# Kernel optimization log

Hardware: AMD Instinct MI355X
Metric: run time of the kernel (lower is better)

The kernel has to match this reference:

```python
import jax, jax.numpy as jnp
import numpy as np

B, C, H, W = 64, 3, 64, 64
F = 96          # base_filters
K = 8           # n_mixtures
h, w = H // 2, W // 2
C0 = 2 * C      # channels of each checkerboard half
SECTIONS = [C0, C0, C0 * K, C0 * K, C0 * K]
SPLITS = [int(s) for s in np.cumsum(SECTIONS)[:-1]]
EPS = 1e-6


def conv2d(x, wgt, b):
    y = jax.lax.conv_general_dilated(x, wgt, (1, 1), 'SAME',
                                     dimension_numbers=('NCHW', 'OIHW', 'NCHW'))
    return y + b[None, :, None, None]


def layer_norm(x, g, b, eps=1e-5):
    # nn.LayerNorm(mid_shape): normalize over (C,H,W) per sample
    mu = jnp.mean(x, axis=(1, 2, 3), keepdims=True)
    var = jnp.var(x, axis=(1, 2, 3), keepdims=True)
    return (x - mu) / jnp.sqrt(var + eps) * g[None] + b[None]


def checker_split(z, odd=False):
    Bz, Cz, Hz, Wz = z.shape
    z = z.reshape(Bz, Cz, Hz // 2, 2, Wz // 2, 2)
    p00 = z[:, :, :, 0, :, 0]; p01 = z[:, :, :, 0, :, 1]
    p10 = z[:, :, :, 1, :, 0]; p11 = z[:, :, :, 1, :, 1]
    z0 = jnp.concatenate([p00, p11], axis=1)  # even checkerboard
    z1 = jnp.concatenate([p01, p10], axis=1)  # odd checkerboard
    if odd:
        z0, z1 = z1, z0
    return z0, z1


def checker_merge(z0, z1, odd=False):
    if odd:
        z0, z1 = z1, z0
    Cz = z0.shape[1] // 2
    p00, p11 = z0[:, :Cz], z0[:, Cz:]
    p01, p10 = z1[:, :Cz], z1[:, Cz:]
    Bz, _, hz, wz = p00.shape
    zi = jnp.stack([jnp.stack([p00, p01], axis=-1),
                    jnp.stack([p10, p11], axis=-1)], axis=-2)  # (B,C,h,w,2i,2j)
    z = zi.transpose(0, 1, 2, 4, 3, 5).reshape(Bz, Cz, 2 * hz, 2 * wz)
    return z


def gated_attn(x, qkv_w, qkv_b, proj_w, proj_b):
    Bx, Fx, hx, wx = x.shape
    xf = x.reshape(Bx, Fx, hx * wx).transpose(0, 2, 1)  # (B, L, F)
    qkv = xf @ qkv_w.T + qkv_b
    q, k, v = jnp.split(qkv, 3, axis=-1)
    scores = jnp.einsum('bqf,bkf->bqk', q, k) / jnp.sqrt(jnp.float32(Fx))
    attn = jax.nn.softmax(scores, axis=-1)
    o = jnp.einsum('bqk,bkf->bqf', attn, v)
    g = o @ proj_w.T + proj_b
    ga, gb = jnp.split(g, 2, axis=-1)
    out = xf + ga * jax.nn.sigmoid(gb)  # gated residual
    return out.transpose(0, 2, 1).reshape(Bx, Fx, hx, wx)


def conditioner(z1, conv1_w, conv1_b, gconv_w, gconv_b, ln1_g, ln1_b,
                qkv_w, qkv_b, proj_w, proj_b, ln2_g, ln2_b, conv2_w, conv2_b):
    x = conv2d(z1, conv1_w, conv1_b)
    g = conv2d(x, gconv_w, gconv_b)
    ga, gb = jnp.split(g, 2, axis=1)
    x = x + ga * jax.nn.sigmoid(gb)          # GatedConv2d
    x = layer_norm(x, ln1_g, ln1_b)
    x = gated_attn(x, qkv_w, qkv_b, proj_w, proj_b)
    x = layer_norm(x, ln2_g, ln2_b)
    return conv2d(x, conv2_w, conv2_b)


def _forward(z, log_df_dz, conv1_w, conv1_b, gconv_w, gconv_b, ln1_g, ln1_b,
             qkv_w, qkv_b, proj_w, proj_b, ln2_g, ln2_b, conv2_w, conv2_b,
             a_log_scale, a_bias):
    z0, z1 = checker_split(z)
    params = conditioner(z1, conv1_w, conv1_b, gconv_w, gconv_b, ln1_g, ln1_b,
                         qkv_w, qkv_b, proj_w, proj_b, ln2_g, ln2_b, conv2_w, conv2_b)
    a, b, logpi, mu, s = jnp.split(params, SPLITS, axis=1)
    a = jnp.tanh(a) * a_log_scale + a_bias
    Bz = z0.shape[0]
    logpi = jax.nn.log_softmax(logpi.reshape(Bz, K, C0, h, w), axis=1)
    mu = mu.reshape(Bz, K, C0, h, w)
    s = s.reshape(Bz, K, C0, h, w)
    # mixture-of-logistics CDF
    u = (z0[:, None] - mu) * jnp.exp(-s)
    x = jnp.sum(jnp.exp(logpi) * jax.nn.sigmoid(u), axis=1)
    log_pdf = jax.scipy.special.logsumexp(
        logpi - s + jax.nn.log_sigmoid(u) + jax.nn.log_sigmoid(-u), axis=1)
    log_df_dz = log_df_dz + jnp.sum(log_pdf.reshape(Bz, -1), axis=1)
    # logit transform
    x = jnp.clip(x, EPS, 1.0 - EPS)
    z0n = jnp.log(x) - jnp.log1p(-x)
    log_df_dz = log_df_dz + jnp.sum((-jnp.log(x) - jnp.log1p(-x)).reshape(Bz, -1), axis=1)
    # affine rescale
    z0n = z0n * jnp.exp(a) + b
    log_df_dz = log_df_dz + jnp.sum(a.reshape(Bz, -1), axis=1)
    return checker_merge(z0n, z1), log_df_dz


def setup_inputs() -> dict:
    key = jax.random.key(0)
    ks = jax.random.split(key, 10)
    sc = 0.05
    return dict(
        z=jax.random.normal(ks[0], (B, C, H, W), jnp.float32),
        log_df_dz=jnp.zeros((B,), jnp.float32),
        conv1_w=sc * jax.random.normal(ks[1], (F, C0, 3, 3), jnp.float32),
        conv1_b=jnp.zeros((F,), jnp.float32),
        gconv_w=sc * jax.random.normal(ks[2], (2 * F, F, 3, 3), jnp.float32),
        gconv_b=jnp.zeros((2 * F,), jnp.float32),
        ln1_g=jnp.ones((F, h, w), jnp.float32),
        ln1_b=jnp.zeros((F, h, w), jnp.float32),
        qkv_w=sc * jax.random.normal(ks[3], (3 * F, F), jnp.float32),
        qkv_b=jnp.zeros((3 * F,), jnp.float32),
        proj_w=sc * jax.random.normal(ks[4], (2 * F, F), jnp.float32),
        proj_b=jnp.zeros((2 * F,), jnp.float32),
        ln2_g=jnp.ones((F, h, w), jnp.float32),
        ln2_b=jnp.zeros((F, h, w), jnp.float32),
        conv2_w=sc * jax.random.normal(ks[5], (sum(SECTIONS), F, 3, 3), jnp.float32),
        conv2_b=jnp.zeros((sum(SECTIONS),), jnp.float32),
        a_log_scale=0.01 * jax.random.normal(ks[6], (1,), jnp.float32),
        a_bias=0.01 * jax.random.normal(ks[7], (1,), jnp.float32),
    )


def reference(z, log_df_dz, conv1_w, conv1_b, gconv_w, gconv_b, ln1_g, ln1_b,
              qkv_w, qkv_b, proj_w, proj_b, ln2_g, ln2_b, conv2_w, conv2_b,
              a_log_scale, a_bias):
    return _forward(z, log_df_dz, conv1_w, conv1_b, gconv_w, gconv_b, ln1_g, ln1_b,
                    qkv_w, qkv_b, proj_w, proj_b, ln2_g, ln2_b, conv2_w, conv2_b,
                    a_log_scale, a_bias)
```

## Files before the change

kernel.cpp:

```cpp
#include <hip/hip_runtime.h>
#include <cstdint>
#include <cstddef>


typedef unsigned short u16;
typedef __attribute__((ext_vector_type(8))) short short8;
typedef __attribute__((ext_vector_type(4))) float f32x4;
typedef __attribute__((ext_vector_type(4))) unsigned int u32x4;

__device__ __forceinline__ float sigm(float x){ return 1.0f/(1.0f+__expf(-x)); }

__device__ __forceinline__ u16 f2bf(float f){
    unsigned int u = __float_as_uint(f);
    u += 0x7fffu + ((u >> 16) & 1u);
    return (u16)(u >> 16);
}
__device__ __forceinline__ float bf2f(u16 v){
    unsigned int u = ((unsigned int)v) << 16;
    return __uint_as_float(u);
}

__device__ __forceinline__ void dma16(const u16* g, u16* l){
    __builtin_amdgcn_global_load_lds(
        (const __attribute__((address_space(1))) void*)g,
        (__attribute__((address_space(3))) void*)l,
        16, 0, 0);
}

__device__ __forceinline__ float ex2(float x){
    float r; asm("v_exp_f32 %0, %1" : "=v"(r) : "v"(x)); return r;
}
__device__ __forceinline__ unsigned cvtpk(float lo, float hi){
    unsigned r; asm("v_cvt_pk_bf16_f32 %0, %1, %2" : "=v"(r) : "v"(lo), "v"(hi)); return r;
}
__device__ __forceinline__ void plswap32(unsigned &a, unsigned &b){
    asm("v_permlane32_swap_b32 %0, %1" : "+v"(a), "+v"(b));
}
__device__ __forceinline__ void plswap16(unsigned &a, unsigned &b){
    asm("v_permlane16_swap_b32 %0, %1" : "+v"(a), "+v"(b));
}

#define SOFTPACK(S, LACC, PA) do { \
    unsigned pk_[4][2]; \
    _Pragma("unroll") \
    for (int t=0;t<4;++t){ \
        float e0 = ex2(S[t][0]); \
        float e1 = ex2(S[t][1]); \
        float e2 = ex2(S[t][2]); \
        float e3 = ex2(S[t][3]); \
        LACC += (e0+e1)+(e2+e3); \
        pk_[t][0] = cvtpk(e0,e1); \
        pk_[t][1] = cvtpk(e2,e3); \
    } \
    _Pragma("unroll") \
    for (int kk=0;kk<2;++kk){ \
        unsigned a0 = pk_[2*kk][0], b0 = pk_[2*kk+1][0]; \
        unsigned a1 = pk_[2*kk][1], b1 = pk_[2*kk+1][1]; \
        plswap32(a0,b0); plswap16(a0,b0); \
        plswap32(a1,b1); plswap16(a1,b1); \
        u32x4 dw_; dw_[0]=a0; dw_[1]=a1; dw_[2]=b0; dw_[3]=b1; \
        PA[kk] = __builtin_bit_cast(short8, dw_); \
    } \
} while(0)

__device__ __forceinline__ short8 ln_frag(const u16* __restrict__ xg,
    const float* __restrict__ gt, const float* __restrict__ bt,
    int p, int c0, float mu, float rr)
{
    short8 x8 = *reinterpret_cast<const short8*>(xg + (size_t)p*96 + c0);
    const float* gp = gt + (size_t)p*96 + c0;
    const float* bp = bt + (size_t)p*96 + c0;
    short8 o;
    #pragma unroll
    for (int j=0;j<8;++j){
        float ag = rr*gp[j];
        o[j] = (short)f2bf(bf2f((u16)x8[j])*ag + (bp[j] - mu*ag));
    }
    return o;
}

__global__ __launch_bounds__(256) void k_prep(
    const float* __restrict__ z, const float* __restrict__ c1w, const float* __restrict__ c1b,
    const float* __restrict__ gw, const float* __restrict__ c2w,
    const float* __restrict__ qkvw, const float* __restrict__ pw,
    const float* __restrict__ ln1g, const float* __restrict__ ln1b,
    const float* __restrict__ ln2g, const float* __restrict__ ln2b,
    const float* __restrict__ logdf,
    u16* __restrict__ x1b,
    u16* __restrict__ Wg, u16* __restrict__ W2,
    u16* __restrict__ Wqkv, u16* __restrict__ Wproj,
    float* __restrict__ gt1, float* __restrict__ bt1,
    float* __restrict__ gt2, float* __restrict__ bt2,
    float* __restrict__ outlog)
{
    int blk = blockIdx.x;
    int tid = threadIdx.x;
    __shared__ float tin[6][6][34];
    __shared__ __align__(16) u16 Wc[96][72];
    __shared__ __align__(16) u16 imc[128][72];

    if (blk < 512){
        int b  = blk >> 3;
        int pg = blk & 7;
        int r0 = pg*4;
        for (int e = tid; e < 96*72; e += 256){
            int oc = e/72, k = e%72;
            Wc[oc][k] = (k < 54) ? f2bf(c1w[oc*54 + k]) : (u16)0;
        }
        for (int idx = tid; idx < 6*6*34; idx += 256){
            int c = idx/204, rem = idx%204;
            int rr = rem/34, q = rem%34;
            int ii = r0 - 1 + rr, jj = q - 1;
            float v = 0.f;
            if ((unsigned)ii < 32u && (unsigned)jj < 32u){
                if (c < 3) v = z[((b*3+c)*64 + 2*ii)*64 + (2*jj+1)];
                else       v = z[((b*3+(c-3))*64 + (2*ii+1))*64 + 2*jj];
            }
            tin[c][rr][q] = v;
        }
        __syncthreads();
        for (int e = tid; e < 128*72; e += 256){
            int px = e/72, k = e%72;
            float v = 0.f;
            if (k < 54){
                int c = k/9, rr = (k%9)/3, dcc = k%3;
                v = tin[c][(px>>5)+rr][(px&31)+dcc];
            }
            imc[px][k] = f2bf(v);
        }
        __syncthreads();

        int w = tid >> 6, lane = tid & 63;
        int cc = lane & 15, gg = lane >> 4;
        f32x4 acc[2][6];
        #pragma unroll
        for (int u=0;u<2;++u)
            #pragma unroll
            for (int t=0;t<6;++t) acc[u][t] = (f32x4){0.f,0.f,0.f,0.f};

        #pragma unroll
        for (int ks=0; ks<2; ++ks){
            short8 a0 = *reinterpret_cast<const short8*>(&imc[w*32 + cc     ][ks*32 + 8*gg]);
            short8 a1 = *reinterpret_cast<const short8*>(&imc[w*32 + 16 + cc][ks*32 + 8*gg]);
            #pragma unroll
            for (int t=0; t<6; ++t){
                short8 bb = *reinterpret_cast<const short8*>(&Wc[t*16+cc][ks*32 + 8*gg]);
                acc[0][t] = __builtin_amdgcn_mfma_f32_16x16x32_bf16(a0, bb, acc[0][t], 0,0,0);
                acc[1][t] = __builtin_amdgcn_mfma_f32_16x16x32_bf16(a1, bb, acc[1][t], 0,0,0);
            }
        }

        #pragma unroll
        for (int u=0;u<2;++u){
            int p0 = pg*128 + w*32 + u*16 + gg*4;
            #pragma unroll
            for (int t=0;t<6;++t){
                int oc = t*16+cc;
                float bv = c1b[oc];
                #pragma unroll
                for (int r=0;r<4;++r)
                    x1b[((size_t)(b*1024) + p0 + r)*96 + oc] = f2bf(acc[u][t][r] + bv);
            }
        }
    } else if (blk < 1160){
        int idx = (blk-512)*256 + tid;
        int j = idx & 7;
        int lane = (idx >> 3) & 63;
        int fo = idx >> 9;
        int frag = fo % 18;
        int tob = fo / 18;
        int obk = tob & 1, tap = tob >> 1;
        int t = frag/3, ks = frag%3;
        int cc = lane & 15, gg = lane >> 4;
        int ocp = obk*96 + t*16 + cc;
        int r2 = ocp%96, isB = r2/48, i2 = r2%48;
        int oc = (ocp/96)*48 + i2 + isB*96;
        int ic = ks*32 + 8*gg + j;
        Wg[idx] = f2bf(gw[(size_t)(oc*96+ic)*9 + tap]);
    } else if (blk < 1700){
        int idx = (blk-1160)*256 + tid;
        int j = idx & 7;
        int lane = (idx >> 3) & 63;
        int fo = idx >> 9;
        int frag = fo % 15;
        int tob = fo / 15;
        int obk = tob & 1, tap = tob >> 1;
        int t = frag/3, ks = frag%3;
        int cc = lane & 15, gg = lane >> 4;
        int oc = obk*80 + t*16 + cc;
        int ic = ks*32 + 8*gg + j;
        W2[idx] = (oc < 156) ? f2bf(c2w[(size_t)(oc*96+ic)*9 + tap]) : (u16)0;
    } else if (blk < 1808){
        int idx = (blk-1700)*256 + tid;
        int j = idx & 7;
        int lane = (idx >> 3) & 63;
        int fo = idx >> 9;
        int frag = fo % 27;
        int obk = fo / 27;
        int t = frag/3, ks = frag%3;
        int cc = lane & 15, gg = lane >> 4;
        int n = obk*144 + t*16 + cc;
        int ic = ks*32 + 8*gg + j;
        Wqkv[idx] = f2bf(qkvw[(size_t)n*96 + ic]);
    } else if (blk < 1880){
        int idx = (blk-1808)*256 + tid;
        int j = idx & 7;
        int lane = (idx >> 3) & 63;
        int fo = idx >> 9;
        int frag = fo % 18;
        int obk = fo / 18;
        int t = frag/3, ks = frag%3;
        int cc = lane & 15, gg = lane >> 4;
        int ocp = obk*96 + t*16 + cc;
        int r2 = ocp%96, isB = r2/48, i2 = r2%48;
        int oc = obk*48 + i2 + isB*96;
        int ic = ks*32 + 8*gg + j;
        Wproj[idx] = f2bf(pw[(size_t)oc*96 + ic]);
    } else if (blk < 2264){
        int idx = (blk-1880)*256 + tid;
        int c = idx >> 10, p = idx & 1023;
        gt1[p*96 + c] = ln1g[idx];
    } else if (blk < 2648){
        int idx = (blk-2264)*256 + tid;
        int c = idx >> 10, p = idx & 1023;
        bt1[p*96 + c] = ln1b[idx];
    } else if (blk < 3032){
        int idx = (blk-2648)*256 + tid;
        int c = idx >> 10, p = idx & 1023;
        gt2[p*96 + c] = ln2g[idx];
    } else if (blk < 3416){
        int idx = (blk-3032)*256 + tid;
        int c = idx >> 10, p = idx & 1023;
        bt2[p*96 + c] = ln2b[idx];
    } else {
        if (tid < 64) outlog[tid] = logdf[tid];
    }
}

__global__ __launch_bounds__(256,4) void k_gconv(const u16* __restrict__ Xpb,
    const u16* __restrict__ Wt, const float* __restrict__ bias,
    u16* __restrict__ outb, float* __restrict__ partials)
{
    int blk  = blockIdx.x;
    int obk  = blk & 1;
    int pblk = (blk >> 1) & 7;
    int b    = blk >> 4;
    int tid  = threadIdx.x;
    int w = tid >> 6, lane = tid & 63;
    int cc = lane & 15, gg = lane >> 4;

    __shared__ __align__(16) u16 Ws[2][9216];
    __shared__ float red[8];

    f32x4 acc[2][6];
    #pragma unroll
    for (int u=0;u<2;++u)
        #pragma unroll
        for (int t=0;t<6;++t) acc[u][t] = (f32x4){0.f,0.f,0.f,0.f};

    int base = pblk*128 + w*32;
    int ia = base >> 5;
    const u16* xb = Xpb + (size_t)b*1024*96;

    {
        const u16* src = Wt + (size_t)obk*9216;
        #pragma unroll
        for (int i=0;i<5;++i){
            int c = tid + 256*i;
            if (c < 1152) dma16(src + (size_t)c*8, Ws[0] + (size_t)(w*64+256*i)*8);
        }
    }

    for (int tap=0; tap<9; ++tap){
        __syncthreads();
        if (tap < 8){
            const u16* src = Wt + (size_t)((tap+1)*2 + obk)*9216;
            int nb = (tap+1)&1;
            #pragma unroll
            for (int i=0;i<5;++i){
                int c = tid + 256*i;
                if (c < 1152) dma16(src + (size_t)c*8, Ws[nb] + (size_t)(w*64+256*i)*8);
            }
        }
        const u16* Wc = Ws[tap&1];
        int dr = tap/3 - 1, dc = tap%3 - 1;

        int ii = ia + dr;
        int jj0 = cc + dc, jj1 = cc + 16 + dc;
        bool rv = ((unsigned)ii < 32u);
        bool v0 = rv && ((unsigned)jj0 < 32u);
        bool v1 = rv && ((unsigned)jj1 < 32u);
        const u16* ar0 = xb + (ptrdiff_t)(ii*32 + jj0)*96 + 8*gg;
        const u16* ar1 = xb + (ptrdiff_t)(ii*32 + jj1)*96 + 8*gg;

        #pragma unroll
        for (int ks=0; ks<3; ++ks){
            short8 a0 = {0,0,0,0,0,0,0,0};
            short8 a1 = {0,0,0,0,0,0,0,0};
            if (v0) a0 = *reinterpret_cast<const short8*>(ar0 + ks*32);
            if (v1) a1 = *reinterpret_cast<const short8*>(ar1 + ks*32);
            #pragma unroll
            for (int t=0; t<6; ++t){
                short8 bb = *reinterpret_cast<const short8*>(Wc + ((size_t)(t*3+ks)*64 + lane)*8);
                acc[0][t] = __builtin_amdgcn_mfma_f32_16x16x32_bf16(a0, bb, acc[0][t], 0,0,0);
                acc[1][t] = __builtin_amdgcn_mfma_f32_16x16x32_bf16(a1, bb, acc[1][t], 0,0,0);
            }
        }
    }

    float s = 0.f, ssq = 0.f;
    #pragma unroll
    for (int u=0;u<2;++u){
        int p0 = base + u*16 + gg*4;
        #pragma unroll
        for (int t=0;t<3;++t){
            int ocA = obk*48 + t*16+cc;
            float ba = bias[ocA], bbv = bias[ocA+96];
            #pragma unroll
            for (int r=0;r<4;++r){
                float res = bf2f(Xpb[((size_t)b*1024 + p0+r)*96 + ocA]);
                float va = acc[u][t][r]   + ba;
                float vb = acc[u][t+3][r] + bbv;
                float v = res + va*sigm(vb);
                outb[((size_t)b*1024 + p0+r)*96 + ocA] = f2bf(v);
                s += v; ssq += v*v;
            }
        }
    }
    #pragma unroll
    for (int o=32;o>0;o>>=1){ s += __shfl_down(s,o,64); ssq += __shfl_down(ssq,o,64); }
    if (lane==0){ red[w]=s; red[4+w]=ssq; }
    __syncthreads();
    if (tid==0){
        int slot = b*16 + pblk*2 + obk;
        partials[slot*2+0] = red[0]+red[1]+red[2]+red[3];
        partials[slot*2+1] = red[4]+red[5]+red[6]+red[7];
    }
}

__global__ __launch_bounds__(256) void k_lne(const u16* __restrict__ xb,
    const float* __restrict__ gt, const float* __restrict__ bt,
    const float* __restrict__ partials, u16* __restrict__ out)
{
    int b = blockIdx.x / 48, rem = blockIdx.x % 48;
    float s=0.f, ss=0.f;
    #pragma unroll
    for (int i=0;i<16;++i){ s += partials[(b*16+i)*2]; ss += partials[(b*16+i)*2+1]; }
    float mu = s/98304.f;
    float r = rsqrtf(ss/98304.f - mu*mu + 1e-5f);

    int e8 = rem*256 + threadIdx.x;
    size_t base = (size_t)b*98304 + (size_t)e8*8;
    short8 x8 = *reinterpret_cast<const short8*>(xb + base);
    const float* gp = gt + e8*8;
    const float* bp = bt + e8*8;
    short8 o8;
    #pragma unroll
    for (int i=0;i<8;++i)
        o8[i] = (short)f2bf((bf2f((u16)x8[i]) - mu)*r*gp[i] + bp[i]);
    *reinterpret_cast<short8*>(out + base) = o8;
}

__global__ __launch_bounds__(256,4) void k_conv2m(const u16* __restrict__ Xpb,
    const u16* __restrict__ Wt, const float* __restrict__ bias,
    u16* __restrict__ out)
{
    int blk  = blockIdx.x;
    int obk  = blk & 1;
    int pblk = (blk >> 1) & 7;
    int b    = blk >> 4;
    int tid  = threadIdx.x;
    int w = tid >> 6, lane = tid & 63;
    int cc = lane & 15, gg = lane >> 4;

    __shared__ __align__(16) u16 Ws[2][7680];

    f32x4 acc[2][5];
    #pragma unroll
    for (int u=0;u<2;++u)
        #pragma unroll
        for (int t=0;t<5;++t) acc[u][t] = (f32x4){0.f,0.f,0.f,0.f};

    int base = pblk*128 + w*32;
    int ia = base >> 5;
    const u16* xb = Xpb + (size_t)b*1024*96;

    {
        const u16* src = Wt + (size_t)obk*7680;
        #pragma unroll
        for (int i=0;i<4;++i){
            int c = tid + 256*i;
            if (c < 960) dma16(src + (size_t)c*8, Ws[0] + (size_t)(w*64+256*i)*8);
        }
    }

    for (int tap=0; tap<9; ++tap){
        __syncthreads();
        if (tap < 8){
            const u16* src = Wt + (size_t)((tap+1)*2 + obk)*7680;
            int nb = (tap+1)&1;
            #pragma unroll
            for (int i=0;i<4;++i){
                int c = tid + 256*i;
                if (c < 960) dma16(src + (size_t)c*8, Ws[nb] + (size_t)(w*64+256*i)*8);
            }
        }
        const u16* Wc = Ws[tap&1];
        int dr = tap/3 - 1, dc = tap%3 - 1;

        int ii = ia + dr;
        int jj0 = cc + dc, jj1 = cc + 16 + dc;
        bool rv = ((unsigned)ii < 32u);
        bool v0 = rv && ((unsigned)jj0 < 32u);
        bool v1 = rv && ((unsigned)jj1 < 32u);
        const u16* ar0 = xb + (ptrdiff_t)(ii*32 + jj0)*96 + 8*gg;
        const u16* ar1 = xb + (ptrdiff_t)(ii*32 + jj1)*96 + 8*gg;

        #pragma unroll
        for (int ks=0; ks<3; ++ks){
            short8 a0 = {0,0,0,0,0,0,0,0};
            short8 a1 = {0,0,0,0,0,0,0,0};
            if (v0) a0 = *reinterpret_cast<const short8*>(ar0 + ks*32);
            if (v1) a1 = *reinterpret_cast<const short8*>(ar1 + ks*32);
            #pragma unroll
            for (int t=0; t<5; ++t){
                short8 bb = *reinterpret_cast<const short8*>(Wc + ((size_t)(t*3+ks)*64 + lane)*8);
                acc[0][t] = __builtin_amdgcn_mfma_f32_16x16x32_bf16(a0, bb, acc[0][t], 0,0,0);
                acc[1][t] = __builtin_amdgcn_mfma_f32_16x16x32_bf16(a1, bb, acc[1][t], 0,0,0);
            }
        }
    }

    #pragma unroll
    for (int u=0;u<2;++u){
        int p0 = base + u*16 + gg*4;
        #pragma unroll
        for (int t=0;t<5;++t){
            int oc = obk*80 + t*16+cc;
            if (oc < 156){
                float bv = bias[oc];
                u16* op = out + ((size_t)b*156 + oc)*1024 + p0;
                #pragma unroll
                for (int r=0;r<4;++r) op[r] = f2bf(acc[u][t][r] + bv);
            }
        }
    }
}

__global__ __launch_bounds__(256,4) void k_qkvm(const u16* __restrict__ Xg,
    const float* __restrict__ gt, const float* __restrict__ bt,
    const float* __restrict__ part,
    const u16* __restrict__ Wt, const float* __restrict__ bias,
    u16* __restrict__ Qb, u16* __restrict__ Kf, u16* __restrict__ Vf)
{
    int blk  = blockIdx.x;
    int obk  = blk & 1;
    int pblk = (blk >> 1) & 7;
    int b    = blk >> 4;
    int tid  = threadIdx.x;
    int w = tid >> 6, lane = tid & 63;
    int cc = lane & 15, gg = lane >> 4;
    const float scale = 0.14724445f;

    __shared__ __align__(16) u16 Ws[13824];
    {
        const u16* src = Wt + (size_t)obk*13824;
        #pragma unroll
        for (int i=0;i<7;++i){
            int c = tid + 256*i;
            if (c < 1728) dma16(src + (size_t)c*8, Ws + (size_t)(w*64+256*i)*8);
        }
    }

    float sS=0.f, sQ=0.f;
    #pragma unroll
    for (int i=0;i<16;++i){ sS += part[(b*16+i)*2]; sQ += part[(b*16+i)*2+1]; }
    float mu = sS/98304.f;
    float rr = rsqrtf(sQ/98304.f - mu*mu + 1e-5f);

    f32x4 acc[2][9];
    #pragma unroll
    for (int u=0;u<2;++u)
        #pragma unroll
        for (int t=0;t<9;++t) acc[u][t] = (f32x4){0.f,0.f,0.f,0.f};

    int base = pblk*128 + w*32;
    const u16* xg = Xg + (size_t)b*1024*96;
    __syncthreads();

    #pragma unroll
    for (int ks=0; ks<3; ++ks){
        int c0 = ks*32 + 8*gg;
        short8 a0 = ln_frag(xg, gt, bt, base+cc,    c0, mu, rr);
        short8 a1 = ln_frag(xg, gt, bt, base+cc+16, c0, mu, rr);
        #pragma unroll
        for (int t=0; t<9; ++t){
            short8 bb = *reinterpret_cast<const short8*>(Ws + ((size_t)(t*3+ks)*64 + lane)*8);
            acc[0][t] = __builtin_amdgcn_mfma_f32_16x16x32_bf16(a0, bb, acc[0][t], 0,0,0);
            acc[1][t] = __builtin_amdgcn_mfma_f32_16x16x32_bf16(a1, bb, acc[1][t], 0,0,0);
        }
    }

    #pragma unroll
    for (int u=0;u<2;++u){
        int p0 = base + u*16 + gg*4;
        #pragma unroll
        for (int t=0;t<9;++t){
            int n = obk*144 + t*16+cc;
            float bv = bias[n];
            #pragma unroll
            for (int r=0;r<4;++r){
                int p = p0 + r;
                float av = acc[u][t][r] + bv;
                if (n < 96){
                    Qb[((size_t)(b*1024+p))*96 + n] = f2bf(av*scale);
                } else if (n < 192){
                    int f = n-96;
                    int jt = p>>6, t16 = (p>>4)&3, ccs = p&15;
                    int ks = f>>5, ggs = (f>>3)&3, j = f&7;
                    Kf[(size_t)(b*16+jt)*6144 + (size_t)(((t16*3+ks)*4+ggs)*16+ccs)*8 + j] = f2bf(av);
                } else {
                    int f = n-192;
                    int jt = p>>6, kl = p&63;
                    int kk = kl>>5, ggs = (kl>>3)&3, j = kl&7;
                    int ft = f>>4, ccs = f&15;
                    Vf[(size_t)(b*16+jt)*6144 + (size_t)(((ft*2+kk)*4+ggs)*16+ccs)*8 + j] = f2bf(av);
                }
            }
        }
    }
}

__global__ __launch_bounds__(256,2) void k_attn(const u16* __restrict__ Qb,
    const u16* __restrict__ Kf, const u16* __restrict__ Vf, u16* __restrict__ Ob)
{
    int qt = blockIdx.x >> 6;
    int b  = blockIdx.x & 63;
    int tid = threadIdx.x;
    int w  = tid >> 6;
    int lane = tid & 63;
    int cc = lane & 15;
    int gg = lane >> 4;

    __shared__ __align__(16) u16 Ks[2][6144];
    __shared__ __align__(16) u16 Vs[2][6144];

    int q0 = qt*128 + w*32;

    short8 qf[2][3];
    {
        const u16* qr0 = Qb + ((size_t)(b*1024 + q0 + cc))*96;
        #pragma unroll
        for (int ks=0; ks<3; ++ks){
            qf[0][ks] = *reinterpret_cast<const short8*>(qr0 + ks*32 + 8*gg);
            qf[1][ks] = *reinterpret_cast<const short8*>(qr0 + (size_t)16*96 + ks*32 + 8*gg);
        }
    }

    f32x4 Oacc[2][6];
    #pragma unroll
    for (int u=0;u<2;++u)
        #pragma unroll
        for (int ft=0; ft<6; ++ft) Oacc[u][ft] = (f32x4){0.f,0.f,0.f,0.f};
    float l_acc[2] = {0.f, 0.f};

    const u16* Kb0 = Kf + (size_t)(b*16)*6144;
    const u16* Vb0 = Vf + (size_t)(b*16)*6144;

    #pragma unroll
    for (int i=0;i<3;++i){
        size_t c8 = (size_t)(tid + 256*i)*8;
        size_t l8 = (size_t)(w*64 + 256*i)*8;
        dma16(Kb0 + c8, Ks[0] + l8);
        dma16(Vb0 + c8, Vs[0] + l8);
    }

    for (int jt=0; jt<16; ++jt){
        __syncthreads();
        if (jt < 15){
            const u16* kn = Kb0 + (size_t)(jt+1)*6144;
            const u16* vn = Vb0 + (size_t)(jt+1)*6144;
            int nb = (jt+1)&1;
            #pragma unroll
            for (int i=0;i<3;++i){
                size_t c8 = (size_t)(tid + 256*i)*8;
                size_t l8 = (size_t)(w*64 + 256*i)*8;
                dma16(kn + c8, Ks[nb] + l8);
                dma16(vn + c8, Vs[nb] + l8);
            }
        }

        const u16* Kc = Ks[jt&1];
        const u16* Vc = Vs[jt&1];

        f32x4 S0[4], S1[4];
        #pragma unroll
        for (int t=0;t<4;++t){ S0[t] = (f32x4){0.f,0.f,0.f,0.f}; S1[t] = (f32x4){0.f,0.f,0.f,0.f}; }

        __builtin_amdgcn_s_setprio(1);
        #pragma unroll
        for (int ks=0; ks<3; ++ks){
            #pragma unroll
            for (int t=0; t<4; ++t){
                short8 kb = *reinterpret_cast<const short8*>(Kc + ((t*3+ks)*64 + lane)*8);
                S0[t] = __builtin_amdgcn_mfma_f32_16x16x32_bf16(kb, qf[0][ks], S0[t], 0,0,0);
                S1[t] = __builtin_amdgcn_mfma_f32_16x16x32_bf16(kb, qf[1][ks], S1[t], 0,0,0);
            }
        }
        __builtin_amdgcn_s_setprio(0);

        short8 pa0[2], pa1[2];
        SOFTPACK(S0, l_acc[0], pa0);
        SOFTPACK(S1, l_acc[1], pa1);

        __builtin_amdgcn_s_setprio(1);
        #pragma unroll
        for (int kk=0; kk<2; ++kk){
            #pragma unroll
            for (int ft=0; ft<6; ++ft){
                short8 vb = *reinterpret_cast<const short8*>(Vc + ((ft*2+kk)*64 + lane)*8);
                Oacc[0][ft] = __builtin_amdgcn_mfma_f32_16x16x32_bf16(pa0[kk], vb, Oacc[0][ft], 0,0,0);
                Oacc[1][ft] = __builtin_amdgcn_mfma_f32_16x16x32_bf16(pa1[kk], vb, Oacc[1][ft], 0,0,0);
            }
        }
        __builtin_amdgcn_s_setprio(0);
    }

    #pragma unroll
    for (int u=0;u<2;++u){
        float lv = l_acc[u];
        lv += __shfl_xor(lv, 16, 64);
        lv += __shfl_xor(lv, 32, 64);
        float linv[4];
        #pragma unroll
        for (int r=0;r<4;++r) linv[r] = 1.0f / __shfl(lv, 4*gg + r, 64);
        #pragma unroll
        for (int ft=0; ft<6; ++ft)
            #pragma unroll
            for (int r=0; r<4; ++r)
                Ob[((size_t)(b*1024 + q0 + u*16 + 4*gg + r))*96 + ft*16 + cc]
                    = f2bf(Oacc[u][ft][r]*linv[r]);
    }
}

__global__ __launch_bounds__(256,4) void k_projm(const u16* __restrict__ Opb,
    const u16* __restrict__ Wt, const float* __restrict__ bias,
    const u16* __restrict__ Xg, const float* __restrict__ gt, const float* __restrict__ bt,
    const float* __restrict__ part1,
    u16* __restrict__ outb, float* __restrict__ partials)
{
    int blk  = blockIdx.x;
    int obk  = blk & 1;
    int pblk = (blk >> 1) & 7;
    int b    = blk >> 4;
    int tid  = threadIdx.x;
    int w = tid >> 6, lane = tid & 63;
    int cc = lane & 15, gg = lane >> 4;

    __shared__ __align__(16) u16 Ws[9216];
    __shared__ float red[8];
    {
        const u16* src = Wt + (size_t)obk*9216;
        #pragma unroll
        for (int i=0;i<5;++i){
            int c = tid + 256*i;
            if (c < 1152) dma16(src + (size_t)c*8, Ws + (size_t)(w*64+256*i)*8);
        }
    }

    float sS=0.f, sQ=0.f;
    #pragma unroll
    for (int i=0;i<16;++i){ sS += part1[(b*16+i)*2]; sQ += part1[(b*16+i)*2+1]; }
    float mu1 = sS/98304.f;
    float rr1 = rsqrtf(sQ/98304.f - mu1*mu1 + 1e-5f);

    f32x4 acc[2][6];
    #pragma unroll
    for (int u=0;u<2;++u)
        #pragma unroll
        for (int t=0;t<6;++t) acc[u][t] = (f32x4){0.f,0.f,0.f,0.f};

    int base = pblk*128 + w*32;
    const u16* xb = Opb + ((size_t)b*1024 + base)*96;
    __syncthreads();

    #pragma unroll
    for (int ks=0; ks<3; ++ks){
        short8 a0 = *reinterpret_cast<const short8*>(xb + (size_t)cc*96      + ks*32 + 8*gg);
        short8 a1 = *reinterpret_cast<const short8*>(xb + (size_t)(cc+16)*96 + ks*32 + 8*gg);
        #pragma unroll
        for (int t=0; t<6; ++t){
            short8 bb = *reinterpret_cast<const short8*>(Ws + ((size_t)(t*3+ks)*64 + lane)*8);
            acc[0][t] = __builtin_amdgcn_mfma_f32_16x16x32_bf16(a0, bb, acc[0][t], 0,0,0);
            acc[1][t] = __builtin_amdgcn_mfma_f32_16x16x32_bf16(a1, bb, acc[1][t], 0,0,0);
        }
    }

    const u16* resb = Xg + (size_t)b*1024*96;
    float s = 0.f, ssq = 0.f;
    #pragma unroll
    for (int u=0;u<2;++u){
        int p0 = base + u*16 + gg*4;
        #pragma unroll
        for (int t=0;t<3;++t){
            int ocA = obk*48 + t*16+cc;
            float ba = bias[ocA], bbv = bias[ocA+96];
            #pragma unroll
            for (int r=0;r<4;++r){
                int pl = p0 + r;
                float ga = acc[u][t][r]   + ba;
                float gb = acc[u][t+3][r] + bbv;
                float xv = bf2f(resb[(size_t)pl*96 + ocA]);
                float res = (xv - mu1)*rr1*gt[(size_t)pl*96 + ocA] + bt[(size_t)pl*96 + ocA];
                float v = res + ga * sigm(gb);
                outb[((size_t)b*1024 + pl)*96 + ocA] = f2bf(v);
                s += v; ssq += v*v;
            }
        }
    }
    #pragma unroll
    for (int o=32;o>0;o>>=1){ s += __shfl_down(s,o,64); ssq += __shfl_down(ssq,o,64); }
    if (lane==0){ red[w]=s; red[4+w]=ssq; }
    __syncthreads();
    if (tid==0){
        int slot = b*16 + pblk*2 + obk;
        partials[slot*2+0] = red[0]+red[1]+red[2]+red[3];
        partials[slot*2+1] = red[4]+red[5]+red[6]+red[7];
    }
}

__global__ __launch_bounds__(256) void k_mix(const float* __restrict__ z,
    const u16* __restrict__ params, const float* __restrict__ a_ls_p,
    const float* __restrict__ a_b_p, float* __restrict__ out_z, float* __restrict__ out_log)
{
    int b = blockIdx.x / 24;
    int rem = blockIdx.x % 24;
    int c0 = rem / 4;
    int pix = (rem & 3)*256 + threadIdx.x;
    int i = pix >> 5, j = pix & 31;
    float als = a_ls_p[0], abv = a_b_p[0];
    const u16* pb = params + (size_t)b*156*1024;
    float logacc = 0.f;

    if (c0 < 3){
        int idx01 = ((b*3+c0)*64 + 2*i)*64 + 2*j+1;
        int idx10 = ((b*3+c0)*64 + 2*i+1)*64 + 2*j;
        out_z[idx01] = z[idx01];
        out_z[idx10] = z[idx10];
    }

    {
        float z0v = (c0<3) ? z[((b*3+c0)*64 + 2*i)*64 + 2*j]
                           : z[((b*3+(c0-3))*64 + 2*i+1)*64 + 2*j+1];
        float a_raw = bf2f(pb[(c0)*1024 + pix]);
        float bco   = bf2f(pb[(6+c0)*1024 + pix]);
        float lp[8], mu[8], sv[8];
        float m1 = -1e30f;
        #pragma unroll
        for (int k=0;k<8;++k){
            lp[k] = bf2f(pb[(12 + k*6 + c0)*1024 + pix]);
            mu[k] = bf2f(pb[(60 + k*6 + c0)*1024 + pix]);
            sv[k] = bf2f(pb[(108 + k*6 + c0)*1024 + pix]);
            m1 = fmaxf(m1, lp[k]);
        }
        float se = 0.f;
        #pragma unroll
        for (int k=0;k<8;++k) se += __expf(lp[k]-m1);
        float lse = m1 + __logf(se);
        float xm = 0.f, mt = -1e30f;
        float t[8];
        #pragma unroll
        for (int k=0;k<8;++k){
            float lpn = lp[k] - lse;
            float u = (z0v - mu[k]) * __expf(-sv[k]);
            float au = fabsf(u);
            xm += __expf(lpn) * (1.f/(1.f+__expf(-u)));
            float lss = -(au + 2.f*log1pf(__expf(-au)));
            float tk = lpn - sv[k] + lss;
            t[k] = tk; mt = fmaxf(mt, tk);
        }
        float se2 = 0.f;
        #pragma unroll
        for (int k=0;k<8;++k) se2 += __expf(t[k]-mt);
        logacc += mt + __logf(se2);
        xm = fminf(fmaxf(xm, 1e-6f), 1.f-1e-6f);
        float lx = __logf(xm), l1x = log1pf(-xm);
        logacc += -lx - l1x;
        float aa = tanhf(a_raw)*als + abv;
        float z0n = (lx - l1x)*__expf(aa) + bco;
        logacc += aa;
        int oidx = (c0<3) ? ((b*3+c0)*64 + 2*i)*64 + 2*j
                          : ((b*3+(c0-3))*64 + 2*i+1)*64 + 2*j+1;
        out_z[oidx] = z0n;
    }

    #pragma unroll
    for (int o=32;o>0;o>>=1) logacc += __shfl_down(logacc, o, 64);
    __shared__ float part[4];
    if ((threadIdx.x&63)==0) part[threadIdx.x>>6] = logacc;
    __syncthreads();
    if (threadIdx.x==0){
        atomicAdd(out_log + b, part[0]+part[1]+part[2]+part[3]);
    }
}

extern "C" void kernel_launch(void* const* d_in, const int* in_sizes, int n_in,
                              void* d_out, int out_size, void* d_ws, size_t ws_size,
                              hipStream_t stream)
{
    const float* z     = (const float*)d_in[0];
    const float* logdf = (const float*)d_in[1];
    const float* c1w   = (const float*)d_in[2];
    const float* c1b   = (const float*)d_in[3];
    const float* gw    = (const float*)d_in[4];
    const float* gcb   = (const float*)d_in[5];
    const float* ln1g  = (const float*)d_in[6];
    const float* ln1b  = (const float*)d_in[7];
    const float* qkvw  = (const float*)d_in[8];
    const float* qkvb  = (const float*)d_in[9];
    const float* pw    = (const float*)d_in[10];
    const float* pbb   = (const float*)d_in[11];
    const float* ln2g  = (const float*)d_in[12];
    const float* ln2b  = (const float*)d_in[13];
    const float* c2w   = (const float*)d_in[14];
    const float* c2b   = (const float*)d_in[15];
    const float* als   = (const float*)d_in[16];
    const float* ab    = (const float*)d_in[17];

    float* out_z   = (float*)d_out;
    float* out_log = out_z + 786432;

    float* ws     = (float*)d_ws;
    u16*   x1b    = (u16*)(ws + 0);
    u16*   xg_b   = (u16*)(ws + 3145728);
    u16*   Kf     = (u16*)(ws + 6291456);
    u16*   Vf     = (u16*)(ws + 9437184);
    u16*   Ob     = (u16*)(ws + 12582912);
    u16*   x2b    = (u16*)(ws + 15728640);
    u16*   Qb     = x1b;
    u16*   xln2b  = Kf;
    u16*   params = (u16*)(ws + 9437184);
    const size_t T = 19660800;
    float* gt1    = ws + T;
    float* bt1    = ws + T + 98304;
    float* gt2    = ws + T + 196608;
    float* bt2    = ws + T + 294912;
    float* part1  = ws + T + 393216;
    float* part2  = ws + T + 395264;
    u16*   Wg     = (u16*)(ws + T + 397568);
    u16*   W2     = (u16*)(ws + T + 480512);
    u16*   Wqkv   = (u16*)(ws + T + 549632);
    u16*   Wproj  = (u16*)(ws + T + 563456);

    k_prep   <<<3417, 256, 0, stream>>>(z, c1w, c1b, gw, c2w, qkvw, pw,
                                        ln1g, ln1b, ln2g, ln2b, logdf,
                                        x1b, Wg, W2, Wqkv, Wproj,
                                        gt1, bt1, gt2, bt2, out_log);
    k_gconv  <<<1024, 256, 0, stream>>>(x1b, Wg, gcb, xg_b, part1);
    k_qkvm   <<<1024, 256, 0, stream>>>(xg_b, gt1, bt1, part1, Wqkv, qkvb, Qb, Kf, Vf);
    k_attn   <<<512, 256, 0, stream>>>(Qb, Kf, Vf, Ob);
    k_projm  <<<1024, 256, 0, stream>>>(Ob, Wproj, pbb, xg_b, gt1, bt1, part1, x2b, part2);
    k_lne    <<<3072, 256, 0, stream>>>(x2b, gt2, bt2, part2, xln2b);
    k_conv2m <<<1024, 256, 0, stream>>>(xln2b, W2, c2b, params);
    k_mix    <<<1536, 256, 0, stream>>>(z, params, als, ab, out_z, out_log);
}
```

Measured before the change: 268.6 us.

## Merge per-stage kernels into two cooperative persistent kernels with grid sync

The seven non-attention stage kernels are turned into device functions and grouped into two persistent cooperative kernels of 1024 blocks that step through the phases with grid-wide barriers. The aim is to cut kernel launch overhead and the gaps between dependent stages. Shared memory becomes one manually carved buffer per block. If the cooperative launch fails, the code falls back to separate per-phase launches. The costs are grid-sync overhead and lower occupancy freedom, because the grid is capped at the co-resident block count.

```diff
diff --git a/kernel.cpp b/kernel.cpp
--- a/kernel.cpp
+++ b/kernel.cpp
@@ -1,6 +1,9 @@
 #include <hip/hip_runtime.h>
+#include <hip/hip_cooperative_groups.h>
 #include <cstdint>
 #include <cstddef>
+
+namespace cg = cooperative_groups;
 
 
 typedef unsigned short u16;
@@ -79,33 +82,32 @@
     return o;
 }
 
-__global__ __launch_bounds__(256) void k_prep(
-    const float* __restrict__ z, const float* __restrict__ c1w, const float* __restrict__ c1b,
-    const float* __restrict__ gw, const float* __restrict__ c2w,
-    const float* __restrict__ qkvw, const float* __restrict__ pw,
-    const float* __restrict__ ln1g, const float* __restrict__ ln1b,
-    const float* __restrict__ ln2g, const float* __restrict__ ln2b,
-    const float* __restrict__ logdf,
-    u16* __restrict__ x1b,
-    u16* __restrict__ Wg, u16* __restrict__ W2,
-    u16* __restrict__ Wqkv, u16* __restrict__ Wproj,
-    float* __restrict__ gt1, float* __restrict__ bt1,
-    float* __restrict__ gt2, float* __restrict__ bt2,
-    float* __restrict__ outlog)
-{
-    int blk = blockIdx.x;
+struct PArgs {
+    const float *z, *c1w, *c1b, *gw, *c2w, *qkvw, *pw;
+    const float *ln1g, *ln1b, *ln2g, *ln2b, *logdf;
+    const float *gcb, *qkvb, *pbb, *c2b, *als, *ab;
+    u16 *x1b, *Wg, *W2, *Wqkv, *Wproj;
+    float *gt1, *bt1, *gt2, *bt2, *part1, *part2;
+    u16 *xg_b, *Qb, *Kf, *Vf, *Ob, *x2b, *xln2b, *params;
+    float *out_z, *out_log;
+};
+
+
+__device__ void prep_unit(int blk, const PArgs& a, unsigned char* smem)
+{
     int tid = threadIdx.x;
-    __shared__ float tin[6][6][34];
-    __shared__ __align__(16) u16 Wc[96][72];
-    __shared__ __align__(16) u16 imc[128][72];
+    float (*tin)[6][34] = (float(*)[6][34])(smem);
+    u16   (*Wc)[72]     = (u16(*)[72])(smem + 4896);
+    u16   (*imc)[72]    = (u16(*)[72])(smem + 4896 + 13824);
 
     if (blk < 512){
+        __syncthreads();
         int b  = blk >> 3;
         int pg = blk & 7;
         int r0 = pg*4;
         for (int e = tid; e < 96*72; e += 256){
             int oc = e/72, k = e%72;
-            Wc[oc][k] = (k < 54) ? f2bf(c1w[oc*54 + k]) : (u16)0;
+            Wc[oc][k] = (k < 54) ? f2bf(a.c1w[oc*54 + k]) : (u16)0;
         }
         for (int idx = tid; idx < 6*6*34; idx += 256){
             int c = idx/204, rem = idx%204;
@@ -113,8 +115,8 @@
             int ii = r0 - 1 + rr, jj = q - 1;
             float v = 0.f;
             if ((unsigned)ii < 32u && (unsigned)jj < 32u){
-                if (c < 3) v = z[((b*3+c)*64 + 2*ii)*64 + (2*jj+1)];
-                else       v = z[((b*3+(c-3))*64 + (2*ii+1))*64 + 2*jj];
+                if (c < 3) v = a.z[((b*3+c)*64 + 2*ii)*64 + (2*jj+1)];
+                else       v = a.z[((b*3+(c-3))*64 + (2*ii+1))*64 + 2*jj];
             }
             tin[c][rr][q] = v;
         }
@@ -156,10 +158,10 @@
             #pragma unroll
             for (int t=0;t<6;++t){
                 int oc = t*16+cc;
-                float bv = c1b[oc];
+                float bv = a.c1b[oc];
                 #pragma unroll
                 for (int r=0;r<4;++r)
-                    x1b[((size_t)(b*1024) + p0 + r)*96 + oc] = f2bf(acc[u][t][r] + bv);
+                    a.x1b[((size_t)(b*1024) + p0 + r)*96 + oc] = f2bf(acc[u][t][r] + bv);
             }
         }
     } else if (blk < 1160){
@@ -176,7 +178,7 @@
         int r2 = ocp%96, isB = r2/48, i2 = r2%48;
         int oc = (ocp/96)*48 + i2 + isB*96;
         int ic = ks*32 + 8*gg + j;
-        Wg[idx] = f2bf(gw[(size_t)(oc*96+ic)*9 + tap]);
+        a.Wg[idx] = f2bf(a.gw[(size_t)(oc*96+ic)*9 + tap]);
     } else if (blk < 1700){
         int idx = (blk-1160)*256 + tid;
         int j = idx & 7;
@@ -189,7 +191,7 @@
         int cc = lane & 15, gg = lane >> 4;
         int oc = obk*80 + t*16 + cc;
         int ic = ks*32 + 8*gg + j;
-        W2[idx] = (oc < 156) ? f2bf(c2w[(size_t)(oc*96+ic)*9 + tap]) : (u16)0;
+        a.W2[idx] = (oc < 156) ? f2bf(a.c2w[(size_t)(oc*96+ic)*9 + tap]) : (u16)0;
     } else if (blk < 1808){
         int idx = (blk-1700)*256 + tid;
         int j = idx & 7;
@@ -201,7 +203,7 @@
         int cc = lane & 15, gg = lane >> 4;
         int n = obk*144 + t*16 + cc;
         int ic = ks*32 + 8*gg + j;
-        Wqkv[idx] = f2bf(qkvw[(size_t)n*96 + ic]);
+        a.Wqkv[idx] = f2bf(a.qkvw[(size_t)n*96 + ic]);
     } else if (blk < 1880){
         int idx = (blk-1808)*256 + tid;
         int j = idx & 7;
@@ -215,33 +217,30 @@
         int r2 = ocp%96, isB = r2/48, i2 = r2%48;
         int oc = obk*48 + i2 + isB*96;
         int ic = ks*32 + 8*gg + j;
-        Wproj[idx] = f2bf(pw[(size_t)oc*96 + ic]);
+        a.Wproj[idx] = f2bf(a.pw[(size_t)oc*96 + ic]);
     } else if (blk < 2264){
         int idx = (blk-1880)*256 + tid;
         int c = idx >> 10, p = idx & 1023;
-        gt1[p*96 + c] = ln1g[idx];
+        a.gt1[p*96 + c] = a.ln1g[idx];
     } else if (blk < 2648){
         int idx = (blk-2264)*256 + tid;
         int c = idx >> 10, p = idx & 1023;
-        bt1[p*96 + c] = ln1b[idx];
+        a.bt1[p*96 + c] = a.ln1b[idx];
     } else if (blk < 3032){
         int idx = (blk-2648)*256 + tid;
         int c = idx >> 10, p = idx & 1023;
-        gt2[p*96 + c] = ln2g[idx];
+        a.gt2[p*96 + c] = a.ln2g[idx];
     } else if (blk < 3416){
         int idx = (blk-3032)*256 + tid;
         int c = idx >> 10, p = idx & 1023;
-        bt2[p*96 + c] = ln2b[idx];
+        a.bt2[p*96 + c] = a.ln2b[idx];
     } else {
-        if (tid < 64) outlog[tid] = logdf[tid];
-    }
-}
-
-__global__ __launch_bounds__(256,4) void k_gconv(const u16* __restrict__ Xpb,
-    const u16* __restrict__ Wt, const float* __restrict__ bias,
-    u16* __restrict__ outb, float* __restrict__ partials)
-{
-    int blk  = blockIdx.x;
+        if (tid < 64) a.out_log[tid] = a.logdf[tid];
+    }
+}
+
+__device__ void gconv_unit(int blk, const PArgs& a, unsigned char* smem)
+{
     int obk  = blk & 1;
     int pblk = (blk >> 1) & 7;
     int b    = blk >> 4;
@@ -249,8 +248,9 @@
     int w = tid >> 6, lane = tid & 63;
     int cc = lane & 15, gg = lane >> 4;
 
-    __shared__ __align__(16) u16 Ws[2][9216];
-    __shared__ float red[8];
+    u16* Ws0 = (u16*)smem;
+    u16* Ws1 = (u16*)(smem + 18432);
+    float* red = (float*)(smem + 36864);
 
     f32x4 acc[2][6];
     #pragma unroll
@@ -260,29 +260,30 @@
 
     int base = pblk*128 + w*32;
     int ia = base >> 5;
-    const u16* xb = Xpb + (size_t)b*1024*96;
+    const u16* xb = a.xg_b;
+    xb = a.x1b + (size_t)b*1024*96;
 
     {
-        const u16* src = Wt + (size_t)obk*9216;
+        const u16* src = a.Wg + (size_t)obk*9216;
         #pragma unroll
         for (int i=0;i<5;++i){
             int c = tid + 256*i;
-            if (c < 1152) dma16(src + (size_t)c*8, Ws[0] + (size_t)(w*64+256*i)*8);
+            if (c < 1152) dma16(src + (size_t)c*8, Ws0 + (size_t)(w*64+256*i)*8);
         }
     }
 
     for (int tap=0; tap<9; ++tap){
         __syncthreads();
         if (tap < 8){
-            const u16* src = Wt + (size_t)((tap+1)*2 + obk)*9216;
-            int nb = (tap+1)&1;
+            const u16* src = a.Wg + (size_t)((tap+1)*2 + obk)*9216;
+            u16* dst = ((tap+1)&1) ? Ws1 : Ws0;
             #pragma unroll
             for (int i=0;i<5;++i){
                 int c = tid + 256*i;
-                if (c < 1152) dma16(src + (size_t)c*8, Ws[nb] + (size_t)(w*64+256*i)*8);
-            }
-        }
-        const u16* Wc = Ws[tap&1];
+                if (c < 1152) dma16(src + (size_t)c*8, dst + (size_t)(w*64+256*i)*8);
+            }
+        }
+        const u16* Wc = (tap&1) ? Ws1 : Ws0;
         int dr = tap/3 - 1, dc = tap%3 - 1;
 
         int ii = ia + dr;
@@ -315,14 +316,14 @@
         #pragma unroll
         for (int t=0;t<3;++t){
             int ocA = obk*48 + t*16+cc;
-            float ba = bias[ocA], bbv = bias[ocA+96];
+            float ba = a.gcb[ocA], bbv = a.gcb[ocA+96];
             #pragma unroll
             for (int r=0;r<4;++r){
-                float res = bf2f(Xpb[((size_t)b*1024 + p0+r)*96 + ocA]);
+                float res = bf2f(a.x1b[((size_t)b*1024 + p0+r)*96 + ocA]);
                 float va = acc[u][t][r]   + ba;
                 float vb = acc[u][t+3][r] + bbv;
                 float v = res + va*sigm(vb);
-                outb[((size_t)b*1024 + p0+r)*96 + ocA] = f2bf(v);
+                a.xg_b[((size_t)b*1024 + p0+r)*96 + ocA] = f2bf(v);
                 s += v; ssq += v*v;
             }
         }
@@ -333,47 +334,203 @@
     __syncthreads();
     if (tid==0){
         int slot = b*16 + pblk*2 + obk;
-        partials[slot*2+0] = red[0]+red[1]+red[2]+red[3];
-        partials[slot*2+1] = red[4]+red[5]+red[6]+red[7];
-    }
-}
-
-__global__ __launch_bounds__(256) void k_lne(const u16* __restrict__ xb,
-    const float* __restrict__ gt, const float* __restrict__ bt,
-    const float* __restrict__ partials, u16* __restrict__ out)
-{
-    int b = blockIdx.x / 48, rem = blockIdx.x % 48;
-    float s=0.f, ss=0.f;
-    #pragma unroll
-    for (int i=0;i<16;++i){ s += partials[(b*16+i)*2]; ss += partials[(b*16+i)*2+1]; }
-    float mu = s/98304.f;
-    float r = rsqrtf(ss/98304.f - mu*mu + 1e-5f);
-
-    int e8 = rem*256 + threadIdx.x;
-    size_t base = (size_t)b*98304 + (size_t)e8*8;
-    short8 x8 = *reinterpret_cast<const short8*>(xb + base);
-    const float* gp = gt + e8*8;
-    const float* bp = bt + e8*8;
-    short8 o8;
-    #pragma unroll
-    for (int i=0;i<8;++i)
-        o8[i] = (short)f2bf((bf2f((u16)x8[i]) - mu)*r*gp[i] + bp[i]);
-    *reinterpret_cast<short8*>(out + base) = o8;
-}
-
-__global__ __launch_bounds__(256,4) void k_conv2m(const u16* __restrict__ Xpb,
-    const u16* __restrict__ Wt, const float* __restrict__ bias,
-    u16* __restrict__ out)
-{
-    int blk  = blockIdx.x;
+        a.part1[slot*2+0] = red[0]+red[1]+red[2]+red[3];
+        a.part1[slot*2+1] = red[4]+red[5]+red[6]+red[7];
+    }
+}
+
+__device__ void qkvm_unit(int blk, const PArgs& a, unsigned char* smem)
+{
     int obk  = blk & 1;
     int pblk = (blk >> 1) & 7;
     int b    = blk >> 4;
     int tid  = threadIdx.x;
     int w = tid >> 6, lane = tid & 63;
     int cc = lane & 15, gg = lane >> 4;
-
-    __shared__ __align__(16) u16 Ws[2][7680];
+    const float scale = 0.14724445f;
+
+    u16* Ws = (u16*)smem;
+    {
+        const u16* src = a.Wqkv + (size_t)obk*13824;
+        #pragma unroll
+        for (int i=0;i<7;++i){
+            int c = tid + 256*i;
+            if (c < 1728) dma16(src + (size_t)c*8, Ws + (size_t)(w*64+256*i)*8);
+        }
+    }
+
+    float sS=0.f, sQ=0.f;
+    #pragma unroll
+    for (int i=0;i<16;++i){ sS += a.part1[(b*16+i)*2]; sQ += a.part1[(b*16+i)*2+1]; }
+    float mu = sS/98304.f;
+    float rr = rsqrtf(sQ/98304.f - mu*mu + 1e-5f);
+
+    f32x4 acc[2][9];
+    #pragma unroll
+    for (int u=0;u<2;++u)
+        #pragma unroll
+        for (int t=0;t<9;++t) acc[u][t] = (f32x4){0.f,0.f,0.f,0.f};
+
+    int base = pblk*128 + w*32;
+    const u16* xg = a.xg_b + (size_t)b*1024*96;
+    __syncthreads();
+
+    #pragma unroll
+    for (int ks=0; ks<3; ++ks){
+        int c0 = ks*32 + 8*gg;
+        short8 a0 = ln_frag(xg, a.gt1, a.bt1, base+cc,    c0, mu, rr);
+        short8 a1 = ln_frag(xg, a.gt1, a.bt1, base+cc+16, c0, mu, rr);
+        #pragma unroll
+        for (int t=0; t<9; ++t){
+            short8 bb = *reinterpret_cast<const short8*>(Ws + ((size_t)(t*3+ks)*64 + lane)*8);
+            acc[0][t] = __builtin_amdgcn_mfma_f32_16x16x32_bf16(a0, bb, acc[0][t], 0,0,0);
+            acc[1][t] = __builtin_amdgcn_mfma_f32_16x16x32_bf16(a1, bb, acc[1][t], 0,0,0);
+        }
+    }
+
+    #pragma unroll
+    for (int u=0;u<2;++u){
+        int p0 = base + u*16 + gg*4;
+        #pragma unroll
+        for (int t=0;t<9;++t){
+            int n = obk*144 + t*16+cc;
+            float bv = a.qkvb[n];
+            #pragma unroll
+            for (int r=0;r<4;++r){
+                int p = p0 + r;
+                float av = acc[u][t][r] + bv;
+                if (n < 96){
+                    a.Qb[((size_t)(b*1024+p))*96 + n] = f2bf(av*scale);
+                } else if (n < 192){
+                    int f = n-96;
+                    int jt = p>>6, t16 = (p>>4)&3, ccs = p&15;
+                    int ks = f>>5, ggs = (f>>3)&3, j = f&7;
+                    a.Kf[(size_t)(b*16+jt)*6144 + (size_t)(((t16*3+ks)*4+ggs)*16+ccs)*8 + j] = f2bf(av);
+                } else {
+                    int f = n-192;
+                    int jt = p>>6, kl = p&63;
+                    int kk = kl>>5, ggs = (kl>>3)&3, j = kl&7;
+                    int ft = f>>4, ccs = f&15;
+                    a.Vf[(size_t)(b*16+jt)*6144 + (size_t)(((ft*2+kk)*4+ggs)*16+ccs)*8 + j] = f2bf(av);
+                }
+            }
+        }
+    }
+}
+
+__device__ void projm_unit(int blk, const PArgs& a, unsigned char* smem)
+{
+    int obk  = blk & 1;
+    int pblk = (blk >> 1) & 7;
+    int b    = blk >> 4;
+    int tid  = threadIdx.x;
+    int w = tid >> 6, lane = tid & 63;
+    int cc = lane & 15, gg = lane >> 4;
+
+    u16* Ws = (u16*)smem;
+    float* red = (float*)(smem + 18432);
+    {
+        const u16* src = a.Wproj + (size_t)obk*9216;
+        #pragma unroll
+        for (int i=0;i<5;++i){
+            int c = tid + 256*i;
+            if (c < 1152) dma16(src + (size_t)c*8, Ws + (size_t)(w*64+256*i)*8);
+        }
+    }
+
+    float sS=0.f, sQ=0.f;
+    #pragma unroll
+    for (int i=0;i<16;++i){ sS += a.part1[(b*16+i)*2]; sQ += a.part1[(b*16+i)*2+1]; }
+    float mu1 = sS/98304.f;
+    float rr1 = rsqrtf(sQ/98304.f - mu1*mu1 + 1e-5f);
+
+    f32x4 acc[2][6];
+    #pragma unroll
+    for (int u=0;u<2;++u)
+        #pragma unroll
+        for (int t=0;t<6;++t) acc[u][t] = (f32x4){0.f,0.f,0.f,0.f};
+
+    int base = pblk*128 + w*32;
+    const u16* xb = a.Ob + ((size_t)b*1024 + base)*96;
+    __syncthreads();
+
+    #pragma unroll
+    for (int ks=0; ks<3; ++ks){
+        short8 a0 = *reinterpret_cast<const short8*>(xb + (size_t)cc*96      + ks*32 + 8*gg);
+        short8 a1 = *reinterpret_cast<const short8*>(xb + (size_t)(cc+16)*96 + ks*32 + 8*gg);
+        #pragma unroll
+        for (int t=0; t<6; ++t){
+            short8 bb = *reinterpret_cast<const short8*>(Ws + ((size_t)(t*3+ks)*64 + lane)*8);
+            acc[0][t] = __builtin_amdgcn_mfma_f32_16x16x32_bf16(a0, bb, acc[0][t], 0,0,0);
+            acc[1][t] = __builtin_amdgcn_mfma_f32_16x16x32_bf16(a1, bb, acc[1][t], 0,0,0);
+        }
+    }
+
+    const u16* resb = a.xg_b + (size_t)b*1024*96;
+    float s = 0.f, ssq = 0.f;
+    #pragma unroll
+    for (int u=0;u<2;++u){
+        int p0 = base + u*16 + gg*4;
+        #pragma unroll
+        for (int t=0;t<3;++t){
+            int ocA = obk*48 + t*16+cc;
+            float ba = a.pbb[ocA], bbv = a.pbb[ocA+96];
+            #pragma unroll
+            for (int r=0;r<4;++r){
+                int pl = p0 + r;
+                float ga = acc[u][t][r]   + ba;
+                float gb = acc[u][t+3][r] + bbv;
+                float xv = bf2f(resb[(size_t)pl*96 + ocA]);
+                float res = (xv - mu1)*rr1*a.gt1[(size_t)pl*96 + ocA] + a.bt1[(size_t)pl*96 + ocA];
+                float v = res + ga * sigm(gb);
+                a.x2b[((size_t)b*1024 + pl)*96 + ocA] = f2bf(v);
+                s += v; ssq += v*v;
+            }
+        }
+    }
+    #pragma unroll
+    for (int o=32;o>0;o>>=1){ s += __shfl_down(s,o,64); ssq += __shfl_down(ssq,o,64); }
+    if (lane==0){ red[w]=s; red[4+w]=ssq; }
+    __syncthreads();
+    if (tid==0){
+        int slot = b*16 + pblk*2 + obk;
+        a.part2[slot*2+0] = red[0]+red[1]+red[2]+red[3];
+        a.part2[slot*2+1] = red[4]+red[5]+red[6]+red[7];
+    }
+}
+
+__device__ void lne2_unit(int u, const PArgs& a)
+{
+    int b = u / 48, rem = u % 48;
+    float s=0.f, ss=0.f;
+    #pragma unroll
+    for (int i=0;i<16;++i){ s += a.part2[(b*16+i)*2]; ss += a.part2[(b*16+i)*2+1]; }
+    float mu = s/98304.f;
+    float r = rsqrtf(ss/98304.f - mu*mu + 1e-5f);
+
+    int e8 = rem*256 + threadIdx.x;
+    size_t base = (size_t)b*98304 + (size_t)e8*8;
+    short8 x8 = *reinterpret_cast<const short8*>(a.x2b + base);
+    const float* gp = a.gt2 + e8*8;
+    const float* bp = a.bt2 + e8*8;
+    short8 o8;
+    #pragma unroll
+    for (int i=0;i<8;++i)
+        o8[i] = (short)f2bf((bf2f((u16)x8[i]) - mu)*r*gp[i] + bp[i]);
+    *reinterpret_cast<short8*>(a.xln2b + base) = o8;
+}
+
+__device__ void conv2m_unit(int blk, const PArgs& a, unsigned char* smem)
+{
+    int obk  = blk & 1;
+    int pblk = (blk >> 1) & 7;
+    int b    = blk >> 4;
+    int tid  = threadIdx.x;
+    int w = tid >> 6, lane = tid & 63;
+    int cc = lane & 15, gg = lane >> 4;
+
+    u16* Ws0 = (u16*)smem;
+    u16* Ws1 = (u16*)(smem + 15360);
 
     f32x4 acc[2][5];
     #pragma unroll
@@ -383,29 +540,29 @@
 
     int base = pblk*128 + w*32;
     int ia = base >> 5;
-    const u16* xb = Xpb + (size_t)b*1024*96;
+    const u16* xb = a.xln2b + (size_t)b*1024*96;
 
     {
-        const u16* src = Wt + (size_t)obk*7680;
+        const u16* src = a.W2 + (size_t)obk*7680;
         #pragma unroll
         for (int i=0;i<4;++i){
             int c = tid + 256*i;
-            if (c < 960) dma16(src + (size_t)c*8, Ws[0] + (size_t)(w*64+256*i)*8);
+            if (c < 960) dma16(src + (size_t)c*8, Ws0 + (size_t)(w*64+256*i)*8);
         }
     }
 
     for (int tap=0; tap<9; ++tap){
         __syncthreads();
         if (tap < 8){
-            const u16* src = Wt + (size_t)((tap+1)*2 + obk)*7680;
-            int nb = (tap+1)&1;
+            const u16* src = a.W2 + (size_t)((tap+1)*2 + obk)*7680;
+            u16* dst = ((tap+1)&1) ? Ws1 : Ws0;
             #pragma unroll
             for (int i=0;i<4;++i){
                 int c = tid + 256*i;
-                if (c < 960) dma16(src + (size_t)c*8, Ws[nb] + (size_t)(w*64+256*i)*8);
-            }
-        }
-        const u16* Wc = Ws[tap&1];
+                if (c < 960) dma16(src + (size_t)c*8, dst + (size_t)(w*64+256*i)*8);
+            }
+        }
+        const u16* Wc = (tap&1) ? Ws1 : Ws0;
         int dr = tap/3 - 1, dc = tap%3 - 1;
 
         int ii = ia + dr;
@@ -438,8 +595,8 @@
         for (int t=0;t<5;++t){
             int oc = obk*80 + t*16+cc;
             if (oc < 156){
-                float bv = bias[oc];
-                u16* op = out + ((size_t)b*156 + oc)*1024 + p0;
+                float bv = a.c2b[oc];
+                u16* op = a.params + ((size_t)b*156 + oc)*1024 + p0;
                 #pragma unroll
                 for (int r=0;r<4;++r) op[r] = f2bf(acc[u][t][r] + bv);
             }
@@ -447,87 +604,117 @@
     }
 }
 
-__global__ __launch_bounds__(256,4) void k_qkvm(const u16* __restrict__ Xg,
-    const float* __restrict__ gt, const float* __restrict__ bt,
-    const float* __restrict__ part,
-    const u16* __restrict__ Wt, const float* __restrict__ bias,
-    u16* __restrict__ Qb, u16* __restrict__ Kf, u16* __restrict__ Vf)
-{
-    int blk  = blockIdx.x;
-    int obk  = blk & 1;
-    int pblk = (blk >> 1) & 7;
-    int b    = blk >> 4;
-    int tid  = threadIdx.x;
-    int w = tid >> 6, lane = tid & 63;
-    int cc = lane & 15, gg = lane >> 4;
-    const float scale = 0.14724445f;
-
-    __shared__ __align__(16) u16 Ws[13824];
-    {
-        const u16* src = Wt + (size_t)obk*13824;
-        #pragma unroll
-        for (int i=0;i<7;++i){
-            int c = tid + 256*i;
-            if (c < 1728) dma16(src + (size_t)c*8, Ws + (size_t)(w*64+256*i)*8);
-        }
-    }
-
-    float sS=0.f, sQ=0.f;
-    #pragma unroll
-    for (int i=0;i<16;++i){ sS += part[(b*16+i)*2]; sQ += part[(b*16+i)*2+1]; }
-    float mu = sS/98304.f;
-    float rr = rsqrtf(sQ/98304.f - mu*mu + 1e-5f);
-
-    f32x4 acc[2][9];
-    #pragma unroll
-    for (int u=0;u<2;++u)
-        #pragma unroll
-        for (int t=0;t<9;++t) acc[u][t] = (f32x4){0.f,0.f,0.f,0.f};
-
-    int base = pblk*128 + w*32;
-    const u16* xg = Xg + (size_t)b*1024*96;
+__device__ __forceinline__ float mix_elem(const PArgs& a, int b, int e)
+{
+    int c0 = e >> 10;
+    int pix = e & 1023;
+    int i = pix >> 5, j = pix & 31;
+    float als = a.als[0], abv = a.ab[0];
+    const u16* pb = a.params + (size_t)b*156*1024;
+    float logacc = 0.f;
+
+    if (c0 < 3){
+        int idx01 = ((b*3+c0)*64 + 2*i)*64 + 2*j+1;
+        int idx10 = ((b*3+c0)*64 + 2*i+1)*64 + 2*j;
+        a.out_z[idx01] = a.z[idx01];
+        a.out_z[idx10] = a.z[idx10];
+    }
+
+    float z0v = (c0<3) ? a.z[((b*3+c0)*64 + 2*i)*64 + 2*j]
+                       : a.z[((b*3+(c0-3))*64 + 2*i+1)*64 + 2*j+1];
+    float a_raw = bf2f(pb[(c0)*1024 + pix]);
+    float bco   = bf2f(pb[(6+c0)*1024 + pix]);
+    float lp[8], mu[8], sv[8];
+    float m1 = -1e30f;
+    #pragma unroll
+    for (int k=0;k<8;++k){
+        lp[k] = bf2f(pb[(12 + k*6 + c0)*1024 + pix]);
+        mu[k] = bf2f(pb[(60 + k*6 + c0)*1024 + pix]);
+        sv[k] = bf2f(pb[(108 + k*6 + c0)*1024 + pix]);
+        m1 = fmaxf(m1, lp[k]);
+    }
+    float se = 0.f;
+    #pragma unroll
+    for (int k=0;k<8;++k) se += __expf(lp[k]-m1);
+    float lse = m1 + __logf(se);
+    float xm = 0.f, mt = -1e30f;
+    float t[8];
+    #pragma unroll
+    for (int k=0;k<8;++k){
+        float lpn = lp[k] - lse;
+        float u = (z0v - mu[k]) * __expf(-sv[k]);
+        float au = fabsf(u);
+        xm += __expf(lpn) * (1.f/(1.f+__expf(-u)));
+        float lss = -(au + 2.f*log1pf(__expf(-au)));
+        float tk = lpn - sv[k] + lss;
+        t[k] = tk; mt = fmaxf(mt, tk);
+    }
+    float se2 = 0.f;
+    #pragma unroll
+    for (int k=0;k<8;++k) se2 += __expf(t[k]-mt);
+    logacc += mt + __logf(se2);
+    xm = fminf(fmaxf(xm, 1e-6f), 1.f-1e-6f);
+    float lx = __logf(xm), l1x = log1pf(-xm);
+    logacc += -lx - l1x;
+    float aa = tanhf(a_raw)*als + abv;
+    float z0n = (lx - l1x)*__expf(aa) + bco;
+    logacc += aa;
+    int oidx = (c0<3) ? ((b*3+c0)*64 + 2*i)*64 + 2*j
+                      : ((b*3+(c0-3))*64 + 2*i+1)*64 + 2*j+1;
+    a.out_z[oidx] = z0n;
+    return logacc;
+}
+
+__device__ void mix_unit(int u, const PArgs& a, float* part)
+{
+    int b = u >> 4, s = u & 15;
+    int tid = threadIdx.x;
+    float logacc = mix_elem(a, b, s*384 + tid);
+    if (tid < 128) logacc += mix_elem(a, b, s*384 + 256 + tid);
+    #pragma unroll
+    for (int o=32;o>0;o>>=1) logacc += __shfl_down(logacc, o, 64);
+    if ((tid&63)==0) part[tid>>6] = logacc;
     __syncthreads();
-
-    #pragma unroll
-    for (int ks=0; ks<3; ++ks){
-        int c0 = ks*32 + 8*gg;
-        short8 a0 = ln_frag(xg, gt, bt, base+cc,    c0, mu, rr);
-        short8 a1 = ln_frag(xg, gt, bt, base+cc+16, c0, mu, rr);
-        #pragma unroll
-        for (int t=0; t<9; ++t){
-            short8 bb = *reinterpret_cast<const short8*>(Ws + ((size_t)(t*3+ks)*64 + lane)*8);
-            acc[0][t] = __builtin_amdgcn_mfma_f32_16x16x32_bf16(a0, bb, acc[0][t], 0,0,0);
-            acc[1][t] = __builtin_amdgcn_mfma_f32_16x16x32_bf16(a1, bb, acc[1][t], 0,0,0);
-        }
-    }
-
-    #pragma unroll
-    for (int u=0;u<2;++u){
-        int p0 = base + u*16 + gg*4;
-        #pragma unroll
-        for (int t=0;t<9;++t){
-            int n = obk*144 + t*16+cc;
-            float bv = bias[n];
-            #pragma unroll
-            for (int r=0;r<4;++r){
-                int p = p0 + r;
-                float av = acc[u][t][r] + bv;
-                if (n < 96){
-                    Qb[((size_t)(b*1024+p))*96 + n] = f2bf(av*scale);
-                } else if (n < 192){
-                    int f = n-96;
-                    int jt = p>>6, t16 = (p>>4)&3, ccs = p&15;
-                    int ks = f>>5, ggs = (f>>3)&3, j = f&7;
-                    Kf[(size_t)(b*16+jt)*6144 + (size_t)(((t16*3+ks)*4+ggs)*16+ccs)*8 + j] = f2bf(av);
-                } else {
-                    int f = n-192;
-                    int jt = p>>6, kl = p&63;
-                    int kk = kl>>5, ggs = (kl>>3)&3, j = kl&7;
-                    int ft = f>>4, ccs = f&15;
-                    Vf[(size_t)(b*16+jt)*6144 + (size_t)(((ft*2+kk)*4+ggs)*16+ccs)*8 + j] = f2bf(av);
-                }
-            }
-        }
+    if (tid==0) atomicAdd(a.out_log + b, part[0]+part[1]+part[2]+part[3]);
+}
+
+__global__ __launch_bounds__(256,4) void k_fused1(PArgs a, int phase)
+{
+    __shared__ __align__(16) unsigned char smem[37152];
+    if (phase < 0){
+        for (unsigned u = blockIdx.x; u < 3417; u += gridDim.x) prep_unit(u, a, smem);
+        cg::this_grid().sync();
+        gconv_unit(blockIdx.x, a, smem);
+        cg::this_grid().sync();
+        qkvm_unit(blockIdx.x, a, smem);
+    } else if (phase == 0){
+        for (unsigned u = blockIdx.x; u < 3417; u += gridDim.x) prep_unit(u, a, smem);
+    } else if (phase == 1){
+        gconv_unit(blockIdx.x, a, smem);
+    } else {
+        qkvm_unit(blockIdx.x, a, smem);
+    }
+}
+
+__global__ __launch_bounds__(256,4) void k_fused2(PArgs a, int phase)
+{
+    __shared__ __align__(16) unsigned char smem[30752];
+    if (phase < 0){
+        projm_unit(blockIdx.x, a, smem);
+        cg::this_grid().sync();
+        for (unsigned u = blockIdx.x; u < 3072; u += gridDim.x) lne2_unit(u, a);
+        cg::this_grid().sync();
+        conv2m_unit(blockIdx.x, a, smem);
+        cg::this_grid().sync();
+        mix_unit(blockIdx.x, a, (float*)smem);
+    } else if (phase == 0){
+        projm_unit(blockIdx.x, a, smem);
+    } else if (phase == 1){
+        for (unsigned u = blockIdx.x; u < 3072; u += gridDim.x) lne2_unit(u, a);
+    } else if (phase == 2){
+        conv2m_unit(blockIdx.x, a, smem);
+    } else {
+        mix_unit(blockIdx.x, a, (float*)smem);
     }
 }
 
@@ -643,224 +830,74 @@
     }
 }
 
-__global__ __launch_bounds__(256,4) void k_projm(const u16* __restrict__ Opb,
-    const u16* __restrict__ Wt, const float* __restrict__ bias,
-    const u16* __restrict__ Xg, const float* __restrict__ gt, const float* __restrict__ bt,
-    const float* __restrict__ part1,
-    u16* __restrict__ outb, float* __restrict__ partials)
-{
-    int blk  = blockIdx.x;
-    int obk  = blk & 1;
-    int pblk = (blk >> 1) & 7;
-    int b    = blk >> 4;
-    int tid  = threadIdx.x;
-    int w = tid >> 6, lane = tid & 63;
-    int cc = lane & 15, gg = lane >> 4;
-
-    __shared__ __align__(16) u16 Ws[9216];
-    __shared__ float red[8];
-    {
-        const u16* src = Wt + (size_t)obk*9216;
-        #pragma unroll
-        for (int i=0;i<5;++i){
-            int c = tid + 256*i;
-            if (c < 1152) dma16(src + (size_t)c*8, Ws + (size_t)(w*64+256*i)*8);
-        }
-    }
-
-    float sS=0.f, sQ=0.f;
-    #pragma unroll
-    for (int i=0;i<16;++i){ sS += part1[(b*16+i)*2]; sQ += part1[(b*16+i)*2+1]; }
-    float mu1 = sS/98304.f;
-    float rr1 = rsqrtf(sQ/98304.f - mu1*mu1 + 1e-5f);
-
-    f32x4 acc[2][6];
-    #pragma unroll
-    for (int u=0;u<2;++u)
-        #pragma unroll
-        for (int t=0;t<6;++t) acc[u][t] = (f32x4){0.f,0.f,0.f,0.f};
-
-    int base = pblk*128 + w*32;
-    const u16* xb = Opb + ((size_t)b*1024 + base)*96;
-    __syncthreads();
-
-    #pragma unroll
-    for (int ks=0; ks<3; ++ks){
-        short8 a0 = *reinterpret_cast<const short8*>(xb + (size_t)cc*96      + ks*32 + 8*gg);
-        short8 a1 = *reinterpret_cast<const short8*>(xb + (size_t)(cc+16)*96 + ks*32 + 8*gg);
-        #pragma unroll
-        for (int t=0; t<6; ++t){
-            short8 bb = *reinterpret_cast<const short8*>(Ws + ((size_t)(t*3+ks)*64 + lane)*8);
-            acc[0][t] = __builtin_amdgcn_mfma_f32_16x16x32_bf16(a0, bb, acc[0][t], 0,0,0);
-            acc[1][t] = __builtin_amdgcn_mfma_f32_16x16x32_bf16(a1, bb, acc[1][t], 0,0,0);
-        }
-    }
-
-    const u16* resb = Xg + (size_t)b*1024*96;
-    float s = 0.f, ssq = 0.f;
-    #pragma unroll
-    for (int u=0;u<2;++u){
-        int p0 = base + u*16 + gg*4;
-        #pragma unroll
-        for (int t=0;t<3;++t){
-            int ocA = obk*48 + t*16+cc;
-            float ba = bias[ocA], bbv = bias[ocA+96];
-            #pragma unroll
-            for (int r=0;r<4;++r){
-                int pl = p0 + r;
-                float ga = acc[u][t][r]   + ba;
-                float gb = acc[u][t+3][r] + bbv;
-                float xv = bf2f(resb[(size_t)pl*96 + ocA]);
-                float res = (xv - mu1)*rr1*gt[(size_t)pl*96 + ocA] + bt[(size_t)pl*96 + ocA];
-                float v = res + ga * sigm(gb);
-                outb[((size_t)b*1024 + pl)*96 + ocA] = f2bf(v);
-                s += v; ssq += v*v;
-            }
-        }
-    }
-    #pragma unroll
-    for (int o=32;o>0;o>>=1){ s += __shfl_down(s,o,64); ssq += __shfl_down(ssq,o,64); }
-    if (lane==0){ red[w]=s; red[4+w]=ssq; }
-    __syncthreads();
-    if (tid==0){
-        int slot = b*16 + pblk*2 + obk;
-        partials[slot*2+0] = red[0]+red[1]+red[2]+red[3];
-        partials[slot*2+1] = red[4]+red[5]+red[6]+red[7];
-    }
-}
-
-__global__ __launch_bounds__(256) void k_mix(const float* __restrict__ z,
-    const u16* __restrict__ params, const float* __restrict__ a_ls_p,
-    const float* __restrict__ a_b_p, float* __restrict__ out_z, float* __restrict__ out_log)
-{
-    int b = blockIdx.x / 24;
-    int rem = blockIdx.x % 24;
-    int c0 = rem / 4;
-    int pix = (rem & 3)*256 + threadIdx.x;
-    int i = pix >> 5, j = pix & 31;
-    float als = a_ls_p[0], abv = a_b_p[0];
-    const u16* pb = params + (size_t)b*156*1024;
-    float logacc = 0.f;
-
-    if (c0 < 3){
-        int idx01 = ((b*3+c0)*64 + 2*i)*64 + 2*j+1;
-        int idx10 = ((b*3+c0)*64 + 2*i+1)*64 + 2*j;
-        out_z[idx01] = z[idx01];
-        out_z[idx10] = z[idx10];
-    }
-
-    {
-        float z0v = (c0<3) ? z[((b*3+c0)*64 + 2*i)*64 + 2*j]
-                           : z[((b*3+(c0-3))*64 + 2*i+1)*64 + 2*j+1];
-        float a_raw = bf2f(pb[(c0)*1024 + pix]);
-        float bco   = bf2f(pb[(6+c0)*1024 + pix]);
-        float lp[8], mu[8], sv[8];
-        float m1 = -1e30f;
-        #pragma unroll
-        for (int k=0;k<8;++k){
-            lp[k] = bf2f(pb[(12 + k*6 + c0)*1024 + pix]);
-            mu[k] = bf2f(pb[(60 + k*6 + c0)*1024 + pix]);
-            sv[k] = bf2f(pb[(108 + k*6 + c0)*1024 + pix]);
-            m1 = fmaxf(m1, lp[k]);
-        }
-        float se = 0.f;
-        #pragma unroll
-        for (int k=0;k<8;++k) se += __expf(lp[k]-m1);
-        float lse = m1 + __logf(se);
-        float xm = 0.f, mt = -1e30f;
-        float t[8];
-        #pragma unroll
-        for (int k=0;k<8;++k){
-            float lpn = lp[k] - lse;
-            float u = (z0v - mu[k]) * __expf(-sv[k]);
-            float au = fabsf(u);
-            xm += __expf(lpn) * (1.f/(1.f+__expf(-u)));
-            float lss = -(au + 2.f*log1pf(__expf(-au)));
-            float tk = lpn - sv[k] + lss;
-            t[k] = tk; mt = fmaxf(mt, tk);
-        }
-        float se2 = 0.f;
-        #pragma unroll
-        for (int k=0;k<8;++k) se2 += __expf(t[k]-mt);
-        logacc += mt + __logf(se2);
-        xm = fminf(fmaxf(xm, 1e-6f), 1.f-1e-6f);
-        float lx = __logf(xm), l1x = log1pf(-xm);
-        logacc += -lx - l1x;
-        float aa = tanhf(a_raw)*als + abv;
-        float z0n = (lx - l1x)*__expf(aa) + bco;
-        logacc += aa;
-        int oidx = (c0<3) ? ((b*3+c0)*64 + 2*i)*64 + 2*j
-                          : ((b*3+(c0-3))*64 + 2*i+1)*64 + 2*j+1;
-        out_z[oidx] = z0n;
-    }
-
-    #pragma unroll
-    for (int o=32;o>0;o>>=1) logacc += __shfl_down(logacc, o, 64);
-    __shared__ float part[4];
-    if ((threadIdx.x&63)==0) part[threadIdx.x>>6] = logacc;
-    __syncthreads();
-    if (threadIdx.x==0){
-        atomicAdd(out_log + b, part[0]+part[1]+part[2]+part[3]);
-    }
-}
-
 extern "C" void kernel_launch(void* const* d_in, const int* in_sizes, int n_in,
                               void* d_out, int out_size, void* d_ws, size_t ws_size,
                               hipStream_t stream)
 {
-    const float* z     = (const float*)d_in[0];
-    const float* logdf = (const float*)d_in[1];
-    const float* c1w   = (const float*)d_in[2];
-    const float* c1b   = (const float*)d_in[3];
-    const float* gw    = (const float*)d_in[4];
-    const float* gcb   = (const float*)d_in[5];
-    const float* ln1g  = (const float*)d_in[6];
-    const float* ln1b  = (const float*)d_in[7];
-    const float* qkvw  = (const float*)d_in[8];
-    const float* qkvb  = (const float*)d_in[9];
-    const float* pw    = (const float*)d_in[10];
-    const float* pbb   = (const float*)d_in[11];
-    const float* ln2g  = (const float*)d_in[12];
-    const float* ln2b  = (const float*)d_in[13];
-    const float* c2w   = (const float*)d_in[14];
-    const float* c2b   = (const float*)d_in[15];
-    const float* als   = (const float*)d_in[16];
-    const float* ab    = (const float*)d_in[17];
-
-    float* out_z   = (float*)d_out;
-    float* out_log = out_z + 786432;
-
-    float* ws     = (float*)d_ws;
-    u16*   x1b    = (u16*)(ws + 0);
-    u16*   xg_b   = (u16*)(ws + 3145728);
-    u16*   Kf     = (u16*)(ws + 6291456);
-    u16*   Vf     = (u16*)(ws + 9437184);
-    u16*   Ob     = (u16*)(ws + 12582912);
-    u16*   x2b    = (u16*)(ws + 15728640);
-    u16*   Qb     = x1b;
-    u16*   xln2b  = Kf;
-    u16*   params = (u16*)(ws + 9437184);
+    PArgs A;
+    A.z     = (const float*)d_in[0];
+    A.logdf = (const float*)d_in[1];
+    A.c1w   = (const float*)d_in[2];
+    A.c1b   = (const float*)d_in[3];
+    A.gw    = (const float*)d_in[4];
+    A.gcb   = (const float*)d_in[5];
+    A.ln1g  = (const float*)d_in[6];
+    A.ln1b  = (const float*)d_in[7];
+    A.qkvw  = (const float*)d_in[8];
+    A.qkvb  = (const float*)d_in[9];
+    A.pw    = (const float*)d_in[10];
+    A.pbb   = (const float*)d_in[11];
+    A.ln2g  = (const float*)d_in[12];
+    A.ln2b  = (const float*)d_in[13];
+    A.c2w   = (const float*)d_in[14];
+    A.c2b   = (const float*)d_in[15];
+    A.als   = (const float*)d_in[16];
+    A.ab    = (const float*)d_in[17];
+
+    A.out_z   = (float*)d_out;
+    A.out_log = A.out_z + 786432;
+
+    float* ws = (float*)d_ws;
+    A.x1b   = (u16*)(ws + 0);
+    A.xg_b  = (u16*)(ws + 3145728);
+    A.Kf    = (u16*)(ws + 6291456);
+    A.Vf    = (u16*)(ws + 9437184);
+    A.Ob    = (u16*)(ws + 12582912);
+    A.x2b   = (u16*)(ws + 15728640);
+    A.Qb    = A.x1b;
+    A.xln2b = A.Kf;
+    A.params= (u16*)(ws + 9437184);
     const size_t T = 19660800;
-    float* gt1    = ws + T;
-    float* bt1    = ws + T + 98304;
-    float* gt2    = ws + T + 196608;
-    float* bt2    = ws + T + 294912;
-    float* part1  = ws + T + 393216;
-    float* part2  = ws + T + 395264;
-    u16*   Wg     = (u16*)(ws + T + 397568);
-    u16*   W2     = (u16*)(ws + T + 480512);
-    u16*   Wqkv   = (u16*)(ws + T + 549632);
-    u16*   Wproj  = (u16*)(ws + T + 563456);
-
-    k_prep   <<<3417, 256, 0, stream>>>(z, c1w, c1b, gw, c2w, qkvw, pw,
-                                        ln1g, ln1b, ln2g, ln2b, logdf,
-                                        x1b, Wg, W2, Wqkv, Wproj,
-                                        gt1, bt1, gt2, bt2, out_log);
-    k_gconv  <<<1024, 256, 0, stream>>>(x1b, Wg, gcb, xg_b, part1);
-    k_qkvm   <<<1024, 256, 0, stream>>>(xg_b, gt1, bt1, part1, Wqkv, qkvb, Qb, Kf, Vf);
-    k_attn   <<<512, 256, 0, stream>>>(Qb, Kf, Vf, Ob);
-    k_projm  <<<1024, 256, 0, stream>>>(Ob, Wproj, pbb, xg_b, gt1, bt1, part1, x2b, part2);
-    k_lne    <<<3072, 256, 0, stream>>>(x2b, gt2, bt2, part2, xln2b);
-    k_conv2m <<<1024, 256, 0, stream>>>(xln2b, W2, c2b, params);
-    k_mix    <<<1536, 256, 0, stream>>>(z, params, als, ab, out_z, out_log);
-}
+    A.gt1   = ws + T;
+    A.bt1   = ws + T + 98304;
+    A.gt2   = ws + T + 196608;
+    A.bt2   = ws + T + 294912;
+    A.part1 = ws + T + 393216;
+    A.part2 = ws + T + 395264;
+    A.Wg    = (u16*)(ws + T + 397568);
+    A.W2    = (u16*)(ws + T + 480512);
+    A.Wqkv  = (u16*)(ws + T + 549632);
+    A.Wproj = (u16*)(ws + T + 563456);
+
+    int phAll = -1;
+    void* p1[] = { (void*)&A, (void*)&phAll };
+
+    hipError_t e1 = hipLaunchCooperativeKernel((const void*)k_fused1,
+                        dim3(1024), dim3(256), p1, 0, stream);
+    if (e1 != hipSuccess){
+        k_fused1<<<3417, 256, 0, stream>>>(A, 0);
+        k_fused1<<<1024, 256, 0, stream>>>(A, 1);
+        k_fused1<<<1024, 256, 0, stream>>>(A, 2);
+    }
+
+    k_attn<<<512, 256, 0, stream>>>(A.Qb, A.Kf, A.Vf, A.Ob);
+
+    hipError_t e2 = hipLaunchCooperativeKernel((const void*)k_fused2,
+                        dim3(1024), dim3(256), p1, 0, stream);
+    if (e2 != hipSuccess){
+        k_fused2<<<1024, 256, 0, stream>>>(A, 0);
+        k_fused2<<<3072, 256, 0, stream>>>(A, 1);
+        k_fused2<<<1024, 256, 0, stream>>>(A, 2);
+        k_fused2<<<1024, 256, 0, stream>>>(A, 3);
+    }
+}
```

After: 952.0 us. 254% more time.
